# Kernel tuning notes

Hardware: AMD Instinct MI355X
Metric: run time of the kernel (lower is better)

The kernel has to match this reference:

```python
import jax, jax.numpy as jnp
import numpy as np

B = 32       # batch_size
N = 8192     # points per set
D = 128      # d_in
LAM = 0.01   # lambda_ ridge regularizer


def setup_inputs() -> dict:
    key = jax.random.key(0)
    x = jax.random.normal(key, (B, N, D), dtype=jnp.float32)
    return {"x": x}


def reference(x):
    Bb, Nn, Dd = x.shape
    # mean-center over the point dim, then batched cov = diffs^T @ diffs / (N-1)
    diffs = x - x.mean(axis=1, keepdims=True)                  # (B, N, D)
    cov = jnp.einsum('bnd,bne->bde', diffs, diffs) / (Nn - 1)  # (B, D, D)
    cov = cov + LAM * jnp.eye(Dd, dtype=x.dtype)
    # torch.unique(dim=1) with generic float data: rows are all distinct,
    # so it reduces to a lexicographic ascending sort of the D rows.
    # jnp.lexsort uses the LAST key as primary -> reverse columns of m.T.
    idx = jax.vmap(lambda m: jnp.lexsort(m.T[::-1]))(cov)      # (B, D)
    sorted_cov = jnp.take_along_axis(cov, idx[:, :, None], axis=1)
    return sorted_cov.reshape(Bb, Dd * Dd)                     # (B, d_out)
```

## Files before the change

### kernel.cpp

```cpp
#include <hip/hip_runtime.h>
#include <hip/hip_bf16.h>

#define DD 128
#define NPTS 8192
#define BBATCH 32
#define BK 64
#define LAM 0.01f

typedef __attribute__((ext_vector_type(8))) short bf16x8;
typedef __attribute__((ext_vector_type(16))) float f32x16;

__device__ __forceinline__ unsigned f2bf_u(float f) {
    unsigned u = __builtin_bit_cast(unsigned, f);
    return (u + 0x7FFFu + ((u >> 16) & 1u)) >> 16;
}
__device__ __forceinline__ float bf2f(unsigned short u) {
    unsigned v = ((unsigned)u) << 16;
    return __builtin_bit_cast(float, v);
}
__device__ __forceinline__ int swz(int d) { return ((d >> 2) ^ d) & 7; }

template<int P>
__global__ __launch_bounds__(512, 4) void gram_stats(
    const float* __restrict__ x, unsigned short* __restrict__ Spart,
    float* __restrict__ CSpart, float* __restrict__ KDpart)
{
    __shared__ short XT[2][DD * BK];
    constexpr int rowsPerBlk = NPTS / P;
    constexpr int T = rowsPerBlk / BK;

    const int blk = blockIdx.x;
    const int b   = blk & 31;
    const int kc  = blk >> 5;
    const int k0g = kc * rowsPerBlk;
    const float* xb = x + (size_t)b * NPTS * DD;

    const int tid    = threadIdx.x;
    const int lane   = tid & 63;
    const int wave   = tid >> 6;
    const int dg     = tid & 31;
    const int rowgrp = tid >> 5;
    const int chunk  = rowgrp >> 1;
    const int wr32   = (wave & 3) * 32;
    const int wc64   = (wave >> 2) * 64;

    f32x16 acc0 = {}; f32x16 acc1 = {};
    float csum[4] = {0.f, 0.f, 0.f, 0.f};
    float kdot[4] = {0.f, 0.f, 0.f, 0.f};
    float4 R0, R1, R2, R3;

    auto issueLoads = [&](int kt) {
        const float4* s = (const float4*)(xb + (size_t)(k0g + kt + rowgrp * 4) * DD) + dg;
        R0 = s[0]; R1 = s[32]; R2 = s[64]; R3 = s[96];
    };
    auto convertStore = [&](int buf) {
        float x00 = __shfl(R0.x, lane & 32);
        float x01 = __shfl(R1.x, lane & 32);
        float x02 = __shfl(R2.x, lane & 32);
        float x03 = __shfl(R3.x, lane & 32);
        float e0[4] = {R0.x, R0.y, R0.z, R0.w};
        float e1[4] = {R1.x, R1.y, R1.z, R1.w};
        float e2[4] = {R2.x, R2.y, R2.z, R2.w};
        float e3[4] = {R3.x, R3.y, R3.z, R3.w};
        short* Xb = XT[buf];
        #pragma unroll
        for (int i = 0; i < 4; ++i) {
            csum[i] += e0[i] + e1[i] + e2[i] + e3[i];
            kdot[i] += x00 * e0[i] + x01 * e1[i] + x02 * e2[i] + x03 * e3[i];
            const int d = 4 * dg + i;
            unsigned u0 = f2bf_u(e0[i]) | (f2bf_u(e1[i]) << 16);
            unsigned u1 = f2bf_u(e2[i]) | (f2bf_u(e3[i]) << 16);
            const int addr = d * BK + ((chunk ^ swz(d)) * 8) + (rowgrp & 1) * 4;
            uint2 v; v.x = u0; v.y = u1;
            *(uint2*)(Xb + addr) = v;
        }
    };

    issueLoads(0);
    convertStore(0);
    __syncthreads();

    for (int t = 0; t < T; ++t) {
        if (t + 1 < T) issueLoads((t + 1) * BK);
        const short* Xb = XT[t & 1];
        #pragma unroll
        for (int ks = 0; ks < BK / 16; ++ks) {
            const int cb = ks * 2 + (lane >> 5);
            const int m = lane & 31;
            const int ad = wr32 + m, b0d = wc64 + m, b1d = wc64 + 32 + m;
            bf16x8 a  = *(const bf16x8*)(Xb + ad  * BK + ((cb ^ swz(ad))  * 8));
            bf16x8 b0 = *(const bf16x8*)(Xb + b0d * BK + ((cb ^ swz(b0d)) * 8));
            bf16x8 b1 = *(const bf16x8*)(Xb + b1d * BK + ((cb ^ swz(b1d)) * 8));
            acc0 = __builtin_amdgcn_mfma_f32_32x32x16_bf16(a, b0, acc0, 0, 0, 0);
            acc1 = __builtin_amdgcn_mfma_f32_32x32x16_bf16(a, b1, acc1, 0, 0, 0);
        }
        if (t + 1 < T) convertStore((t + 1) & 1);
        __syncthreads();
    }

    unsigned short* Sp = Spart + ((size_t)b * P + kc) * (DD * DD);
    const int colLane = lane & 31;
    const int rowHw = 4 * (lane >> 5);
    #pragma unroll
    for (int r = 0; r < 16; ++r) {
        const int row = wr32 + (r & 3) + 8 * (r >> 2) + rowHw;
        Sp[row * DD + wc64 + colLane]      = (unsigned short)f2bf_u(acc0[r]);
        Sp[row * DD + wc64 + 32 + colLane] = (unsigned short)f2bf_u(acc1[r]);
    }

    __syncthreads();
    float* red = (float*)XT;
    #pragma unroll
    for (int i = 0; i < 4; ++i) {
        red[tid] = csum[i];
        __syncthreads();
        if (tid < 32) {
            float s = 0.f;
            #pragma unroll
            for (int g = 0; g < 16; ++g) s += red[g * 32 + tid];
            CSpart[((size_t)b * P + kc) * DD + 4 * tid + i] = s;
        }
        __syncthreads();
        red[tid] = kdot[i];
        __syncthreads();
        if (tid < 32) {
            float s = 0.f;
            #pragma unroll
            for (int g = 0; g < 16; ++g) s += red[g * 32 + tid];
            KDpart[((size_t)b * P + kc) * DD + 4 * tid + i] = s;
        }
        __syncthreads();
    }
}

template<int P>
__global__ __launch_bounds__(128) void keys_ranks(
    const float* __restrict__ CSpart, const float* __restrict__ KDpart,
    float* __restrict__ csOut, int* __restrict__ rankOut)
{
    __shared__ float csh[DD];
    __shared__ float key[DD];
    const int b = blockIdx.x;
    const int tid = threadIdx.x;
    float s = 0.f, kd = 0.f;
    #pragma unroll
    for (int p = 0; p < P; ++p) {
        s  += CSpart[((size_t)b * P + p) * DD + tid];
        kd += KDpart[((size_t)b * P + p) * DD + tid];
    }
    csh[tid] = s;
    __syncthreads();
    const float k = (kd - s * csh[0] * (1.f / NPTS)) * (1.f / (NPTS - 1))
                  + ((tid == 0) ? LAM : 0.f);
    key[tid] = k;
    __syncthreads();
    int r = 0;
    #pragma unroll 8
    for (int j = 0; j < DD; ++j) {
        const float kj = key[j];
        r += (kj < k) || (kj == k && j < tid);
    }
    csOut[b * DD + tid] = s;
    rankOut[b * DD + tid] = r;
}

template<int P>
__global__ __launch_bounds__(256) void reduce_scatter(
    const unsigned short* __restrict__ Spart, const float* __restrict__ csOut,
    const int* __restrict__ rankOut, float* __restrict__ out)
{
    __shared__ float csh[DD];
    __shared__ int rk[8];
    const int b = blockIdx.x;
    const int seg = blockIdx.y;
    const int tid = threadIdx.x;
    if (tid < DD) csh[tid] = csOut[b * DD + tid];
    if (tid < 8)  rk[tid] = rankOut[b * DD + seg * 8 + tid];

    const int base = seg * (8 * DD) + tid * 4;
    float a0 = 0.f, a1 = 0.f, a2 = 0.f, a3 = 0.f;
    #pragma unroll
    for (int p = 0; p < P; ++p) {
        uint2 v = *(const uint2*)(Spart + ((size_t)b * P + p) * (DD * DD) + base);
        a0 += bf2f((unsigned short)(v.x & 0xFFFFu));
        a1 += bf2f((unsigned short)(v.x >> 16));
        a2 += bf2f((unsigned short)(v.y & 0xFFFFu));
        a3 += bf2f((unsigned short)(v.y >> 16));
    }
    __syncthreads();
    const int row = seg * 8 + (tid >> 5);
    const int j0  = (tid & 31) * 4;
    const float ci = csh[row];
    const float invN = 1.f / NPTS, invNm1 = 1.f / (NPTS - 1);
    float4 v;
    v.x = (a0 - ci * csh[j0 + 0] * invN) * invNm1 + ((row == j0 + 0) ? LAM : 0.f);
    v.y = (a1 - ci * csh[j0 + 1] * invN) * invNm1 + ((row == j0 + 1) ? LAM : 0.f);
    v.z = (a2 - ci * csh[j0 + 2] * invN) * invNm1 + ((row == j0 + 2) ? LAM : 0.f);
    v.w = (a3 - ci * csh[j0 + 3] * invN) * invNm1 + ((row == j0 + 3) ? LAM : 0.f);
    float* o = out + (size_t)b * DD * DD + (size_t)rk[tid >> 5] * DD + j0;
    *(float4*)o = v;
}

template<int P>
static void launch_all(const float* x, float* out, void* d_ws, hipStream_t stream)
{
    size_t nS = (size_t)BBATCH * P * DD * DD;
    unsigned short* Spart = (unsigned short*)d_ws;
    float* CSpart = (float*)(Spart + nS);
    float* KDpart = CSpart + (size_t)BBATCH * P * DD;
    float* csOut  = KDpart + (size_t)BBATCH * P * DD;
    int*   rankOut = (int*)(csOut + (size_t)BBATCH * DD);

    gram_stats<P><<<dim3(32 * P), dim3(512), 0, stream>>>(x, Spart, CSpart, KDpart);
    keys_ranks<P><<<dim3(BBATCH), dim3(128), 0, stream>>>(CSpart, KDpart, csOut, rankOut);
    reduce_scatter<P><<<dim3(BBATCH, 16), dim3(256), 0, stream>>>(Spart, csOut, rankOut, out);
}

extern "C" void kernel_launch(void* const* d_in, const int* in_sizes, int n_in,
                              void* d_out, int out_size, void* d_ws, size_t ws_size,
                              hipStream_t stream)
{
    const float* x = (const float*)d_in[0];
    float* out = (float*)d_out;

    auto need = [](int P) {
        return (size_t)BBATCH * P * DD * DD * sizeof(unsigned short)
             + (size_t)BBATCH * P * 2 * DD * sizeof(float)
             + (size_t)BBATCH * DD * (sizeof(float) + sizeof(int));
    };
    if (need(16) <= ws_size)      launch_all<16>(x, out, d_ws, stream);
    else                          launch_all<8>(x, out, d_ws, stream);
}
```

Baseline: 199.9 us.

## Fuse key/rank kernel into reduce-scatter and batch block-level stat reductions

Removes the separate keys_ranks launch. Each reduce_scatter block (now 512 threads covering 16 rows) recomputes the column sums, diagonal keys and the ranks for its own rows. The gram_stats epilogue also writes all csum/kdot partials to shared memory at once and reduces them behind a single barrier, replacing eight barrier-separated rounds. In exchange, every reduce_scatter block redundantly re-reads the CS/KD partials and recomputes the keys, and the grid shrinks from 512 to 256 blocks.

```diff
diff --git a/kernel.cpp b/kernel.cpp
--- a/kernel.cpp
+++ b/kernel.cpp
@@ -108,76 +108,51 @@
         Sp[row * DD + wc64 + 32 + colLane] = (unsigned short)f2bf_u(acc1[r]);
     }
 
-    __syncthreads();
     float* red = (float*)XT;
     #pragma unroll
     for (int i = 0; i < 4; ++i) {
-        red[tid] = csum[i];
-        __syncthreads();
-        if (tid < 32) {
+        red[i * 512 + tid]       = csum[i];
+        red[(4 + i) * 512 + tid] = kdot[i];
+    }
+    __syncthreads();
+    if (tid < 64) {
+        const int tt = tid & 31;
+        const float* basep = red + ((tid < 32) ? 0 : 4 * 512);
+        float* dst = ((tid < 32) ? CSpart : KDpart) + ((size_t)b * P + kc) * DD;
+        #pragma unroll
+        for (int i = 0; i < 4; ++i) {
             float s = 0.f;
             #pragma unroll
-            for (int g = 0; g < 16; ++g) s += red[g * 32 + tid];
-            CSpart[((size_t)b * P + kc) * DD + 4 * tid + i] = s;
-        }
-        __syncthreads();
-        red[tid] = kdot[i];
-        __syncthreads();
-        if (tid < 32) {
-            float s = 0.f;
-            #pragma unroll
-            for (int g = 0; g < 16; ++g) s += red[g * 32 + tid];
-            KDpart[((size_t)b * P + kc) * DD + 4 * tid + i] = s;
-        }
-        __syncthreads();
+            for (int g = 0; g < 16; ++g) s += basep[i * 512 + g * 32 + tt];
+            dst[4 * tt + i] = s;
+        }
     }
 }
 
 template<int P>
-__global__ __launch_bounds__(128) void keys_ranks(
-    const float* __restrict__ CSpart, const float* __restrict__ KDpart,
-    float* __restrict__ csOut, int* __restrict__ rankOut)
+__global__ __launch_bounds__(512) void reduce_scatter(
+    const unsigned short* __restrict__ Spart, const float* __restrict__ CSpart,
+    const float* __restrict__ KDpart, float* __restrict__ out)
 {
     __shared__ float csh[DD];
     __shared__ float key[DD];
-    const int b = blockIdx.x;
-    const int tid = threadIdx.x;
-    float s = 0.f, kd = 0.f;
-    #pragma unroll
-    for (int p = 0; p < P; ++p) {
-        s  += CSpart[((size_t)b * P + p) * DD + tid];
-        kd += KDpart[((size_t)b * P + p) * DD + tid];
-    }
-    csh[tid] = s;
-    __syncthreads();
-    const float k = (kd - s * csh[0] * (1.f / NPTS)) * (1.f / (NPTS - 1))
-                  + ((tid == 0) ? LAM : 0.f);
-    key[tid] = k;
-    __syncthreads();
-    int r = 0;
-    #pragma unroll 8
-    for (int j = 0; j < DD; ++j) {
-        const float kj = key[j];
-        r += (kj < k) || (kj == k && j < tid);
-    }
-    csOut[b * DD + tid] = s;
-    rankOut[b * DD + tid] = r;
-}
-
-template<int P>
-__global__ __launch_bounds__(256) void reduce_scatter(
-    const unsigned short* __restrict__ Spart, const float* __restrict__ csOut,
-    const int* __restrict__ rankOut, float* __restrict__ out)
-{
-    __shared__ float csh[DD];
-    __shared__ int rk[8];
-    const int b = blockIdx.x;
+    __shared__ int rk[16];
+    const int b   = blockIdx.x;
     const int seg = blockIdx.y;
     const int tid = threadIdx.x;
-    if (tid < DD) csh[tid] = csOut[b * DD + tid];
-    if (tid < 8)  rk[tid] = rankOut[b * DD + seg * 8 + tid];
-
-    const int base = seg * (8 * DD) + tid * 4;
+
+    float kd = 0.f;
+    if (tid < DD) {
+        float s = 0.f;
+        #pragma unroll
+        for (int p = 0; p < P; ++p) {
+            s  += CSpart[((size_t)b * P + p) * DD + tid];
+            kd += KDpart[((size_t)b * P + p) * DD + tid];
+        }
+        csh[tid] = s;
+    }
+
+    const int base = seg * (16 * DD) + tid * 4;
     float a0 = 0.f, a1 = 0.f, a2 = 0.f, a3 = 0.f;
     #pragma unroll
     for (int p = 0; p < P; ++p) {
@@ -188,16 +163,34 @@
         a3 += bf2f((unsigned short)(v.y >> 16));
     }
     __syncthreads();
-    const int row = seg * 8 + (tid >> 5);
-    const int j0  = (tid & 31) * 4;
+    if (tid < DD) {
+        key[tid] = (kd - csh[tid] * csh[0] * (1.f / NPTS)) * (1.f / (NPTS - 1))
+                 + ((tid == 0) ? LAM : 0.f);
+    }
+    __syncthreads();
+    if (tid < 16) {
+        const int j0 = seg * 16 + tid;
+        const float k = key[j0];
+        int r = 0;
+        #pragma unroll 8
+        for (int j = 0; j < DD; ++j) {
+            const float kj = key[j];
+            r += (kj < k) || (kj == k && j < j0);
+        }
+        rk[tid] = r;
+    }
+    __syncthreads();
+
+    const int row = seg * 16 + (tid >> 5);
+    const int c0  = (tid & 31) * 4;
     const float ci = csh[row];
     const float invN = 1.f / NPTS, invNm1 = 1.f / (NPTS - 1);
     float4 v;
-    v.x = (a0 - ci * csh[j0 + 0] * invN) * invNm1 + ((row == j0 + 0) ? LAM : 0.f);
-    v.y = (a1 - ci * csh[j0 + 1] * invN) * invNm1 + ((row == j0 + 1) ? LAM : 0.f);
-    v.z = (a2 - ci * csh[j0 + 2] * invN) * invNm1 + ((row == j0 + 2) ? LAM : 0.f);
-    v.w = (a3 - ci * csh[j0 + 3] * invN) * invNm1 + ((row == j0 + 3) ? LAM : 0.f);
-    float* o = out + (size_t)b * DD * DD + (size_t)rk[tid >> 5] * DD + j0;
+    v.x = (a0 - ci * csh[c0 + 0] * invN) * invNm1 + ((row == c0 + 0) ? LAM : 0.f);
+    v.y = (a1 - ci * csh[c0 + 1] * invN) * invNm1 + ((row == c0 + 1) ? LAM : 0.f);
+    v.z = (a2 - ci * csh[c0 + 2] * invN) * invNm1 + ((row == c0 + 2) ? LAM : 0.f);
+    v.w = (a3 - ci * csh[c0 + 3] * invN) * invNm1 + ((row == c0 + 3) ? LAM : 0.f);
+    float* o = out + (size_t)b * DD * DD + (size_t)rk[tid >> 5] * DD + c0;
     *(float4*)o = v;
 }
 
@@ -208,12 +201,9 @@
     unsigned short* Spart = (unsigned short*)d_ws;
     float* CSpart = (float*)(Spart + nS);
     float* KDpart = CSpart + (size_t)BBATCH * P * DD;
-    float* csOut  = KDpart + (size_t)BBATCH * P * DD;
-    int*   rankOut = (int*)(csOut + (size_t)BBATCH * DD);
 
     gram_stats<P><<<dim3(32 * P), dim3(512), 0, stream>>>(x, Spart, CSpart, KDpart);
-    keys_ranks<P><<<dim3(BBATCH), dim3(128), 0, stream>>>(CSpart, KDpart, csOut, rankOut);
-    reduce_scatter<P><<<dim3(BBATCH, 16), dim3(256), 0, stream>>>(Spart, csOut, rankOut, out);
+    reduce_scatter<P><<<dim3(BBATCH, 8), dim3(512), 0, stream>>>(Spart, CSpart, KDpart, out);
 }
 
 extern "C" void kernel_launch(void* const* d_in, const int* in_sizes, int n_in,
@@ -225,8 +215,7 @@
 
     auto need = [](int P) {
         return (size_t)BBATCH * P * DD * DD * sizeof(unsigned short)
-             + (size_t)BBATCH * P * 2 * DD * sizeof(float)
-             + (size_t)BBATCH * DD * (sizeof(float) + sizeof(int));
+             + (size_t)BBATCH * P * 2 * DD * sizeof(float);
     };
     if (need(16) <= ws_size)      launch_all<16>(x, out, d_ws, stream);
     else                          launch_all<8>(x, out, d_ws, stream);
```

Result: no change. 196.9 us (-1.5%).
